# Performance work log

Hardware: AMD Instinct MI355X
Metric: run time of the kernel (lower is better)

The kernel has to match this reference:

```python
import jax, jax.numpy as jnp
import numpy as np

FP8_MAX = 448.0  # float8_e4m3fn max
EPS = 1e-6
H = 4096
T = 16384


def _rmsnorm(x, w, eps=EPS):
    # vLLM RMSNorm: x * rsqrt(mean(x^2) + eps) * weight, computed in fp32
    ms = jnp.mean(x * x, axis=-1, keepdims=True)
    return x * jax.lax.rsqrt(ms + eps) * w


def _fp8_linear_dyn(y, w_t, wscale):
    # per-token dynamic fp8 quant: scale = max|y| / 448, quantize, fp8 GEMM, dequant
    s = jnp.max(jnp.abs(y), axis=-1, keepdims=True) / FP8_MAX  # [T,1]
    s = jnp.maximum(s, 1e-10)
    q = jnp.clip(y / s, -FP8_MAX, FP8_MAX)
    q = q.astype(jnp.float8_e4m3fn).astype(jnp.float32)  # snap to fp8 grid
    out = q @ w_t                                         # [T,H]
    return out * s * wscale[:, 0]                          # per-token * per-out-channel


def setup_inputs() -> dict:
    key = jax.random.key(0)
    ks = jax.random.split(key, 9)
    x = jax.random.uniform(ks[0], (T, H), dtype=jnp.float32)
    # RMSNorm weights (init ones in vLLM; perturb for a nontrivial baseline)
    nw0 = 1.0 + 0.1 * jax.random.normal(ks[1], (H,), dtype=jnp.float32)
    nw1 = 1.0 + 0.1 * jax.random.normal(ks[2], (H,), dtype=jnp.float32)
    nw2 = 1.0 + 0.1 * jax.random.normal(ks[3], (H,), dtype=jnp.float32)
    # fp8 weights: rand(H,H) snapped to e4m3 grid, transposed (y @ W.T)
    def fp8_w(k):
        w = jax.random.uniform(k, (H, H), dtype=jnp.float32)
        return w.astype(jnp.float8_e4m3fn).astype(jnp.float32).T
    w0 = fp8_w(ks[4])
    w1 = fp8_w(ks[5])
    ws0 = jax.random.uniform(ks[6], (H, 1), dtype=jnp.float32)
    ws1 = jax.random.uniform(ks[7], (H, 1), dtype=jnp.float32)
    return {"x": x, "nw0": nw0, "nw1": nw1, "nw2": nw2,
            "w0": w0, "w1": w1, "ws0": ws0, "ws1": ws1}


def reference(x, nw0, nw1, nw2, w0, w1, ws0, ws1):
    resid = jnp.sqrt(x)
    y = _rmsnorm(x, nw0)
    x2 = _fp8_linear_dyn(y, w0, ws0)
    # fused add + rmsnorm: residual updated in place semantics
    resid = x2 + resid
    y2 = _rmsnorm(resid, nw1)
    x3 = _fp8_linear_dyn(y2, w1, ws1)
    resid = x3 + resid
    y3 = _rmsnorm(resid, nw2)
    return y3
```

## Files before the change

### kernel.cpp

```cpp
#include <hip/hip_runtime.h>
#include <stdint.h>

#define TT 16384
#define HH 4096

typedef uint8_t u8;
typedef uint32_t u32;
typedef __attribute__((ext_vector_type(16))) float f32x16;
typedef __attribute__((ext_vector_type(8))) int i32x8;

__device__ __forceinline__ u32 cvt4_fp8(float a, float b, float c, float d) {
  u32 v = 0;
  v = __builtin_amdgcn_cvt_pk_fp8_f32(a, b, v, false);
  v = __builtin_amdgcn_cvt_pk_fp8_f32(c, d, v, true);
  return v;
}

__device__ __forceinline__ void gl_lds16(const void* g, void* l) {
  __builtin_amdgcn_global_load_lds(
      (const __attribute__((address_space(1))) void*)g,
      (__attribute__((address_space(3))) void*)l, 16, 0, 0);
}

__device__ __forceinline__ i32x8 ld32B(const u8* p0, const u8* p1) {
  const uint4 a = *(const uint4*)p0;
  const uint4 b = *(const uint4*)p1;
  i32x8 r;
  r[0] = (int)a.x; r[1] = (int)a.y; r[2] = (int)a.z; r[3] = (int)a.w;
  r[4] = (int)b.x; r[5] = (int)b.y; r[6] = (int)b.z; r[7] = (int)b.w;
  return r;
}

__global__ __launch_bounds__(256) void kwquant(const float* __restrict__ w,
                                               u8* __restrict__ wq) {
  __shared__ __align__(16) u8 tile[64][68];
  const int n0 = blockIdx.x * 64;
  const int k0 = blockIdx.y * 64;
  const int t = threadIdx.x;
  const int tr = t >> 4, tc = t & 15;
#pragma unroll
  for (int p = 0; p < 4; ++p) {
    const int kl = p * 16 + tr;
    const float4 v = *(const float4*)(w + (size_t)(k0 + kl) * HH + n0 + tc * 4);
    const u32 pk = cvt4_fp8(v.x, v.y, v.z, v.w);
    tile[tc * 4 + 0][kl] = (u8)(pk);
    tile[tc * 4 + 1][kl] = (u8)(pk >> 8);
    tile[tc * 4 + 2][kl] = (u8)(pk >> 16);
    tile[tc * 4 + 3][kl] = (u8)(pk >> 24);
  }
  __syncthreads();
  const int jr = t >> 2;
  const int kc = (t & 3) * 16;
  uint4 ov;
  ov.x = *(const u32*)&tile[jr][kc + 0];
  ov.y = *(const u32*)&tile[jr][kc + 4];
  ov.z = *(const u32*)&tile[jr][kc + 8];
  ov.w = *(const u32*)&tile[jr][kc + 12];
  *(uint4*)(wq + (size_t)(n0 + jr) * HH + k0 + kc) = ov;
}

__device__ __forceinline__ float wred_sum(float v) {
#pragma unroll
  for (int o = 32; o; o >>= 1) v += __shfl_down(v, o, 64);
  return v;
}
__device__ __forceinline__ float wred_max(float v) {
#pragma unroll
  for (int o = 32; o; o >>= 1) v = fmaxf(v, __shfl_down(v, o, 64));
  return v;
}

template <int MODE>
__global__ __launch_bounds__(256) void knorm(const float* __restrict__ src,
                                             const float* __restrict__ nw,
                                             float* __restrict__ resid_out,
                                             u8* __restrict__ qout,
                                             float* __restrict__ sout,
                                             float* __restrict__ yout) {
  __shared__ float red[4];
  __shared__ float redm[4];
  const int row = blockIdx.x;
  const int t = threadIdx.x;
  const int lane = t & 63, wid = t >> 6;
  const float* rp = src + (size_t)row * HH;

  float4 xv[4];
  float ssq = 0.f;
#pragma unroll
  for (int p = 0; p < 4; ++p) {
    xv[p] = *((const float4*)rp + p * 256 + t);
    ssq += xv[p].x * xv[p].x;
    ssq += xv[p].y * xv[p].y;
    ssq += xv[p].z * xv[p].z;
    ssq += xv[p].w * xv[p].w;
  }
  if (MODE == 0) {
    float* rr = resid_out + (size_t)row * HH;
#pragma unroll
    for (int p = 0; p < 4; ++p) {
      float4 r4;
      r4.x = sqrtf(xv[p].x); r4.y = sqrtf(xv[p].y);
      r4.z = sqrtf(xv[p].z); r4.w = sqrtf(xv[p].w);
      *((float4*)rr + p * 256 + t) = r4;
    }
  }
  ssq = wred_sum(ssq);
  if (lane == 0) red[wid] = ssq;
  __syncthreads();
  const float ms = (((red[0] + red[1]) + red[2]) + red[3]) * (1.0f / HH);
  const float inv = 1.0f / sqrtf(ms + 1e-6f);

  float y[16];
  float amax = 0.f;
#pragma unroll
  for (int p = 0; p < 4; ++p) {
    const float4 wv = *((const float4*)nw + p * 256 + t);
    y[p * 4 + 0] = (xv[p].x * inv) * wv.x;
    y[p * 4 + 1] = (xv[p].y * inv) * wv.y;
    y[p * 4 + 2] = (xv[p].z * inv) * wv.z;
    y[p * 4 + 3] = (xv[p].w * inv) * wv.w;
    amax = fmaxf(amax, fabsf(y[p * 4 + 0]));
    amax = fmaxf(amax, fabsf(y[p * 4 + 1]));
    amax = fmaxf(amax, fabsf(y[p * 4 + 2]));
    amax = fmaxf(amax, fabsf(y[p * 4 + 3]));
  }

  if (MODE == 2) {
    float* yp = yout + (size_t)row * HH;
#pragma unroll
    for (int p = 0; p < 4; ++p) {
      float4 o;
      o.x = y[p * 4 + 0]; o.y = y[p * 4 + 1];
      o.z = y[p * 4 + 2]; o.w = y[p * 4 + 3];
      *((float4*)yp + p * 256 + t) = o;
    }
    return;
  }

  amax = wred_max(amax);
  if (lane == 0) redm[wid] = amax;
  __syncthreads();
  const float bmax = fmaxf(fmaxf(redm[0], redm[1]), fmaxf(redm[2], redm[3]));
  const float sval = fmaxf(bmax / 448.0f, 1e-10f);

  u32* qp = (u32*)(qout + (size_t)row * HH);
#pragma unroll
  for (int p = 0; p < 4; ++p) {
    float q0 = fminf(fmaxf(y[p * 4 + 0] / sval, -448.f), 448.f);
    float q1 = fminf(fmaxf(y[p * 4 + 1] / sval, -448.f), 448.f);
    float q2 = fminf(fmaxf(y[p * 4 + 2] / sval, -448.f), 448.f);
    float q3 = fminf(fmaxf(y[p * 4 + 3] / sval, -448.f), 448.f);
    qp[p * 256 + t] = cvt4_fp8(q0, q1, q2, q3);
  }
  if (t == 0) sout[row] = sval;
}

__global__ __launch_bounds__(512) void kgemm(const u8* __restrict__ Aq,
                                             const u8* __restrict__ Bq,
                                             const float* __restrict__ srow,
                                             const float* __restrict__ wsc,
                                             float* __restrict__ resid) {
  constexpr int K = HH, N = HH;
  constexpr int NT = K / 64;
  __shared__ __align__(16) u8 smA[2][256 * 64];
  __shared__ __align__(16) u8 smB[2][256 * 64];

  const int nwg = (TT / 256) * (HH / 256);
  int bid = blockIdx.x;
  bid = (bid & 7) * (nwg >> 3) + (bid >> 3);
  const int tm = bid >> 4;
  const int tn = bid & 15;
  const int row0 = tm * 256, col0 = tn * 256;

  const int t = threadIdx.x;
  const int lane = t & 63, wid = t >> 6;
  const int wm = wid >> 2, wn = wid & 3;
  const int rl32 = lane & 31, hi = lane >> 5;

  f32x16 acc[4][2];
#pragma unroll
  for (int m = 0; m < 4; ++m)
#pragma unroll
    for (int n = 0; n < 2; ++n) acc[m][n] = (f32x16)0.f;

  int aoffg[2], boffg[2], ldso[2];
#pragma unroll
  for (int p = 0; p < 2; ++p) {
    const int s = t + p * 512;
    const int r = s >> 2;
    const int cb = (s & 3) ^ ((r >> 1) & 3);
    aoffg[p] = (row0 + r) * K + cb * 16;
    boffg[p] = (col0 + r) * K + cb * 16;
    ldso[p] = s * 16;
  }

  int aro[4][2], bro[2][2];
#pragma unroll
  for (int m = 0; m < 4; ++m) {
    const int r = wm * 128 + m * 32 + rl32;
    const int swz = (r >> 1) & 3;
    aro[m][0] = r * 64 + ((hi * 2) ^ swz) * 16;
    aro[m][1] = r * 64 + ((hi * 2 + 1) ^ swz) * 16;
  }
#pragma unroll
  for (int n = 0; n < 2; ++n) {
    const int r = wn * 64 + n * 32 + rl32;
    const int swz = (r >> 1) & 3;
    bro[n][0] = r * 64 + ((hi * 2) ^ swz) * 16;
    bro[n][1] = r * 64 + ((hi * 2 + 1) ^ swz) * 16;
  }

#pragma unroll
  for (int p = 0; p < 2; ++p) {
    gl_lds16(Aq + aoffg[p], smA[0] + ldso[p]);
    gl_lds16(Bq + boffg[p], smB[0] + ldso[p]);
  }

  for (int it = 0; it < NT; ++it) {
    if (it + 1 < NT) {
      const size_t ko = (size_t)(it + 1) * 64;
      const int nb = (it + 1) & 1;
#pragma unroll
      for (int p = 0; p < 2; ++p) {
        gl_lds16(Aq + aoffg[p] + ko, smA[nb] + ldso[p]);
        gl_lds16(Bq + boffg[p] + ko, smB[nb] + ldso[p]);
      }
      asm volatile("s_waitcnt vmcnt(4)" ::: "memory");
    } else {
      asm volatile("s_waitcnt vmcnt(0)" ::: "memory");
    }
    __builtin_amdgcn_s_barrier();
    __builtin_amdgcn_sched_barrier(0);

    const u8* sA = smA[it & 1];
    const u8* sB = smB[it & 1];
    const i32x8 bv0 = ld32B(sB + bro[0][0], sB + bro[0][1]);
    const i32x8 bv1 = ld32B(sB + bro[1][0], sB + bro[1][1]);
#pragma unroll
    for (int m = 0; m < 4; ++m) {
      const i32x8 av = ld32B(sA + aro[m][0], sA + aro[m][1]);
      acc[m][0] = __builtin_amdgcn_mfma_scale_f32_32x32x64_f8f6f4(
          av, bv0, acc[m][0], 0 , 0 ,
          0, 0x7f7f7f7f, 0, 0x7f7f7f7f);
      acc[m][1] = __builtin_amdgcn_mfma_scale_f32_32x32x64_f8f6f4(
          av, bv1, acc[m][1], 0, 0, 0, 0x7f7f7f7f, 0, 0x7f7f7f7f);
    }
    __builtin_amdgcn_sched_barrier(0);
    __builtin_amdgcn_s_barrier();
  }

  const int cc = rl32;
  const int rb = hi * 4;
  float wvv[2];
#pragma unroll
  for (int n = 0; n < 2; ++n) wvv[n] = wsc[col0 + wn * 64 + n * 32 + cc];
#pragma unroll
  for (int m = 0; m < 4; ++m) {
#pragma unroll
    for (int g = 0; g < 4; ++g) {
#pragma unroll
      for (int j = 0; j < 4; ++j) {
        const int row = row0 + wm * 128 + m * 32 + g * 8 + rb + j;
        const float sv = srow[row];
#pragma unroll
        for (int n = 0; n < 2; ++n) {
          const int col = col0 + wn * 64 + n * 32 + cc;
          const size_t idx = (size_t)row * N + col;
          resid[idx] = resid[idx] + (acc[m][n][g * 4 + j] * sv) * wvv[n];
        }
      }
    }
  }
}

extern "C" void kernel_launch(void* const* d_in, const int* in_sizes, int n_in,
                              void* d_out, int out_size, void* d_ws, size_t ws_size,
                              hipStream_t stream) {
  const float* x   = (const float*)d_in[0];
  const float* nw0 = (const float*)d_in[1];
  const float* nw1 = (const float*)d_in[2];
  const float* nw2 = (const float*)d_in[3];
  const float* w0  = (const float*)d_in[4];
  const float* w1  = (const float*)d_in[5];
  const float* ws0 = (const float*)d_in[6];
  const float* ws1 = (const float*)d_in[7];
  float* out = (float*)d_out;

  u8* q = (u8*)d_ws;
  u8* w0q = q + (size_t)TT * HH;
  u8* w1q = w0q + (size_t)HH * HH;
  float* sbuf = (float*)(w1q + (size_t)HH * HH);

  dim3 wg(HH / 64, HH / 64);
  kwquant<<<wg, 256, 0, stream>>>(w0, w0q);
  kwquant<<<wg, 256, 0, stream>>>(w1, w1q);

  const int gblocks = (TT / 256) * (HH / 256);
  knorm<0><<<TT, 256, 0, stream>>>(x, nw0, out, q, sbuf, nullptr);
  kgemm<<<gblocks, 512, 0, stream>>>(q, w0q, sbuf, ws0, out);
  knorm<1><<<TT, 256, 0, stream>>>(out, nw1, nullptr, q, sbuf, nullptr);
  kgemm<<<gblocks, 512, 0, stream>>>(q, w1q, sbuf, ws1, out);
  knorm<2><<<TT, 256, 0, stream>>>(out, nw2, nullptr, nullptr, nullptr, out);
}
```

Baseline: 1.109 ms.

## Triple-buffer GEMM LDS and interleave global prefetch with MFMA phases

Replaces the double-buffered A/B shared-memory tiles with a three-stage ring buffer that prefetches two K-steps ahead. Global-to-LDS loads are split into four pieces, each issued inside one of four MFMA sub-phases with barriers and s_setprio around the matrix ops, so memory traffic overlaps compute. The workgroup-to-tile mapping is also changed to group 2x2 tile blocks per XCD for better L2 locality. In exchange it uses more LDS (96KB) and many more barriers per iteration, which could hurt occupancy or add sync overhead.

```diff
diff --git a/kernel.cpp b/kernel.cpp
--- a/kernel.cpp
+++ b/kernel.cpp
@@ -162,14 +162,16 @@
                                              float* __restrict__ resid) {
   constexpr int K = HH, N = HH;
   constexpr int NT = K / 64;
-  __shared__ __align__(16) u8 smA[2][256 * 64];
-  __shared__ __align__(16) u8 smB[2][256 * 64];
-
-  const int nwg = (TT / 256) * (HH / 256);
-  int bid = blockIdx.x;
-  bid = (bid & 7) * (nwg >> 3) + (bid >> 3);
-  const int tm = bid >> 4;
-  const int tn = bid & 15;
+  __shared__ __align__(16) u8 sm[3][32768];
+
+  const int bidraw = blockIdx.x;
+  const int xcd = bidraw & 7;
+  const int c = bidraw >> 3;
+  const int g = c >> 2;
+  const int gr = g >> 3, gc = g & 7;
+  const int gm = (c >> 1) & 1, gn = c & 1;
+  const int tm = xcd * 8 + gr * 2 + gm;
+  const int tn = gc * 2 + gn;
   const int row0 = tm * 256, col0 = tn * 256;
 
   const int t = threadIdx.x;
@@ -183,24 +185,21 @@
 #pragma unroll
     for (int n = 0; n < 2; ++n) acc[m][n] = (f32x16)0.f;
 
-  int aoffg[2], boffg[2], ldso[2];
-#pragma unroll
-  for (int p = 0; p < 2; ++p) {
-    const int s = t + p * 512;
-    const int r = s >> 2;
-    const int cb = (s & 3) ^ ((r >> 1) & 3);
-    aoffg[p] = (row0 + r) * K + cb * 16;
-    boffg[p] = (col0 + r) * K + cb * 16;
-    ldso[p] = s * 16;
-  }
+  const int sr = t >> 2;
+  const int scb = (t & 3) ^ ((sr >> 1) & 3);
+  const int gBlo = (col0 + sr) * K + scb * 16;
+  const int gBhi = (col0 + 128 + sr) * K + scb * 16;
+  const int gAlo = (row0 + sr) * K + scb * 16;
+  const int gAhi = (row0 + 128 + sr) * K + scb * 16;
+  const int dst = t * 16;
 
   int aro[4][2], bro[2][2];
 #pragma unroll
   for (int m = 0; m < 4; ++m) {
     const int r = wm * 128 + m * 32 + rl32;
     const int swz = (r >> 1) & 3;
-    aro[m][0] = r * 64 + ((hi * 2) ^ swz) * 16;
-    aro[m][1] = r * 64 + ((hi * 2 + 1) ^ swz) * 16;
+    aro[m][0] = 16384 + r * 64 + ((hi * 2) ^ swz) * 16;
+    aro[m][1] = 16384 + r * 64 + ((hi * 2 + 1) ^ swz) * 16;
   }
 #pragma unroll
   for (int n = 0; n < 2; ++n) {
@@ -210,43 +209,96 @@
     bro[n][1] = r * 64 + ((hi * 2 + 1) ^ swz) * 16;
   }
 
-#pragma unroll
-  for (int p = 0; p < 2; ++p) {
-    gl_lds16(Aq + aoffg[p], smA[0] + ldso[p]);
-    gl_lds16(Bq + boffg[p], smB[0] + ldso[p]);
-  }
+  gl_lds16(Bq + gBlo, sm[0] + dst);
+  gl_lds16(Bq + gBhi, sm[0] + 8192 + dst);
+  gl_lds16(Aq + gAlo, sm[0] + 16384 + dst);
+  gl_lds16(Aq + gAhi, sm[0] + 24576 + dst);
+  gl_lds16(Bq + gBlo + 64, sm[1] + dst);
+  gl_lds16(Bq + gBhi + 64, sm[1] + 8192 + dst);
+  gl_lds16(Aq + gAlo + 64, sm[1] + 16384 + dst);
+  gl_lds16(Aq + gAhi + 64, sm[1] + 24576 + dst);
+  asm volatile("s_waitcnt vmcnt(4)" ::: "memory");
+  __builtin_amdgcn_s_barrier();
+  __builtin_amdgcn_sched_barrier(0);
 
   for (int it = 0; it < NT; ++it) {
-    if (it + 1 < NT) {
-      const size_t ko = (size_t)(it + 1) * 64;
-      const int nb = (it + 1) & 1;
-#pragma unroll
-      for (int p = 0; p < 2; ++p) {
-        gl_lds16(Aq + aoffg[p] + ko, smA[nb] + ldso[p]);
-        gl_lds16(Bq + boffg[p] + ko, smB[nb] + ldso[p]);
+    const u8* sb = sm[it % 3];
+    u8* db = sm[(it + 2) % 3];
+    const bool st = (it + 2 < NT);
+    const int ko = (it + 2) * 64;
+    i32x8 bv0, bv1;
+
+    {
+      bv0 = ld32B(sb + bro[0][0], sb + bro[0][1]);
+      bv1 = ld32B(sb + bro[1][0], sb + bro[1][1]);
+      const i32x8 av = ld32B(sb + aro[0][0], sb + aro[0][1]);
+      if (st) gl_lds16(Bq + gBlo + ko, db + dst);
+      __builtin_amdgcn_sched_barrier(0);
+      __builtin_amdgcn_s_barrier();
+      asm volatile("s_waitcnt lgkmcnt(0)" ::: "memory");
+      __builtin_amdgcn_sched_barrier(0);
+      __builtin_amdgcn_s_setprio(1);
+      acc[0][0] = __builtin_amdgcn_mfma_scale_f32_32x32x64_f8f6f4(
+          av, bv0, acc[0][0], 0, 0, 0, 0x7f7f7f7f, 0, 0x7f7f7f7f);
+      acc[0][1] = __builtin_amdgcn_mfma_scale_f32_32x32x64_f8f6f4(
+          av, bv1, acc[0][1], 0, 0, 0, 0x7f7f7f7f, 0, 0x7f7f7f7f);
+      __builtin_amdgcn_s_setprio(0);
+      __builtin_amdgcn_sched_barrier(0);
+      __builtin_amdgcn_s_barrier();
+    }
+    {
+      const i32x8 av = ld32B(sb + aro[1][0], sb + aro[1][1]);
+      if (st) gl_lds16(Bq + gBhi + ko, db + 8192 + dst);
+      __builtin_amdgcn_sched_barrier(0);
+      __builtin_amdgcn_s_barrier();
+      asm volatile("s_waitcnt lgkmcnt(0)" ::: "memory");
+      __builtin_amdgcn_sched_barrier(0);
+      __builtin_amdgcn_s_setprio(1);
+      acc[1][0] = __builtin_amdgcn_mfma_scale_f32_32x32x64_f8f6f4(
+          av, bv0, acc[1][0], 0, 0, 0, 0x7f7f7f7f, 0, 0x7f7f7f7f);
+      acc[1][1] = __builtin_amdgcn_mfma_scale_f32_32x32x64_f8f6f4(
+          av, bv1, acc[1][1], 0, 0, 0, 0x7f7f7f7f, 0, 0x7f7f7f7f);
+      __builtin_amdgcn_s_setprio(0);
+      __builtin_amdgcn_sched_barrier(0);
+      __builtin_amdgcn_s_barrier();
+    }
+    {
+      const i32x8 av = ld32B(sb + aro[2][0], sb + aro[2][1]);
+      if (st) gl_lds16(Aq + gAlo + ko, db + 16384 + dst);
+      __builtin_amdgcn_sched_barrier(0);
+      __builtin_amdgcn_s_barrier();
+      asm volatile("s_waitcnt lgkmcnt(0)" ::: "memory");
+      __builtin_amdgcn_sched_barrier(0);
+      __builtin_amdgcn_s_setprio(1);
+      acc[2][0] = __builtin_amdgcn_mfma_scale_f32_32x32x64_f8f6f4(
+          av, bv0, acc[2][0], 0, 0, 0, 0x7f7f7f7f, 0, 0x7f7f7f7f);
+      acc[2][1] = __builtin_amdgcn_mfma_scale_f32_32x32x64_f8f6f4(
+          av, bv1, acc[2][1], 0, 0, 0, 0x7f7f7f7f, 0, 0x7f7f7f7f);
+      __builtin_amdgcn_s_setprio(0);
+      __builtin_amdgcn_sched_barrier(0);
+      __builtin_amdgcn_s_barrier();
+    }
+    {
+      const i32x8 av = ld32B(sb + aro[3][0], sb + aro[3][1]);
+      if (st) gl_lds16(Aq + gAhi + ko, db + 24576 + dst);
+      __builtin_amdgcn_sched_barrier(0);
+      __builtin_amdgcn_s_barrier();
+      asm volatile("s_waitcnt lgkmcnt(0)" ::: "memory");
+      __builtin_amdgcn_sched_barrier(0);
+      __builtin_amdgcn_s_setprio(1);
+      acc[3][0] = __builtin_amdgcn_mfma_scale_f32_32x32x64_f8f6f4(
+          av, bv0, acc[3][0], 0, 0, 0, 0x7f7f7f7f, 0, 0x7f7f7f7f);
+      acc[3][1] = __builtin_amdgcn_mfma_scale_f32_32x32x64_f8f6f4(
+          av, bv1, acc[3][1], 0, 0, 0, 0x7f7f7f7f, 0, 0x7f7f7f7f);
+      __builtin_amdgcn_s_setprio(0);
+      if (st) {
+        asm volatile("s_waitcnt vmcnt(4)" ::: "memory");
+      } else {
+        asm volatile("s_waitcnt vmcnt(0)" ::: "memory");
       }
-      asm volatile("s_waitcnt vmcnt(4)" ::: "memory");
-    } else {
-      asm volatile("s_waitcnt vmcnt(0)" ::: "memory");
-    }
-    __builtin_amdgcn_s_barrier();
-    __builtin_amdgcn_sched_barrier(0);
-
-    const u8* sA = smA[it & 1];
-    const u8* sB = smB[it & 1];
-    const i32x8 bv0 = ld32B(sB + bro[0][0], sB + bro[0][1]);
-    const i32x8 bv1 = ld32B(sB + bro[1][0], sB + bro[1][1]);
-#pragma unroll
-    for (int m = 0; m < 4; ++m) {
-      const i32x8 av = ld32B(sA + aro[m][0], sA + aro[m][1]);
-      acc[m][0] = __builtin_amdgcn_mfma_scale_f32_32x32x64_f8f6f4(
-          av, bv0, acc[m][0], 0 , 0 ,
-          0, 0x7f7f7f7f, 0, 0x7f7f7f7f);
-      acc[m][1] = __builtin_amdgcn_mfma_scale_f32_32x32x64_f8f6f4(
-          av, bv1, acc[m][1], 0, 0, 0, 0x7f7f7f7f, 0, 0x7f7f7f7f);
-    }
-    __builtin_amdgcn_sched_barrier(0);
-    __builtin_amdgcn_s_barrier();
+      __builtin_amdgcn_sched_barrier(0);
+      __builtin_amdgcn_s_barrier();
+    }
   }
 
   const int cc = rl32;
@@ -257,16 +309,16 @@
 #pragma unroll
   for (int m = 0; m < 4; ++m) {
 #pragma unroll
-    for (int g = 0; g < 4; ++g) {
+    for (int g2 = 0; g2 < 4; ++g2) {
 #pragma unroll
       for (int j = 0; j < 4; ++j) {
-        const int row = row0 + wm * 128 + m * 32 + g * 8 + rb + j;
+        const int row = row0 + wm * 128 + m * 32 + g2 * 8 + rb + j;
         const float sv = srow[row];
 #pragma unroll
         for (int n = 0; n < 2; ++n) {
           const int col = col0 + wn * 64 + n * 32 + cc;
           const size_t idx = (size_t)row * N + col;
-          resid[idx] = resid[idx] + (acc[m][n][g * 4 + j] * sv) * wvv[n];
+          resid[idx] = resid[idx] + (acc[m][n][g2 * 4 + j] * sv) * wvv[n];
         }
       }
     }
```

Measured after the change: 1.216 ms. +9.6%, slower.

## Retile FP8 GEMM to 128x128 blocks with triple-buffered LDS pipeline

Applied to the files above, without the earlier changes.

Replaces the 256x256 tile, 8-wave GEMM with a 128x128 tile, 2-wave block. Loads are triple buffered with a prefetch distance of two k-steps. The block-to-tile mapping now groups tiles by XCD for L2 locality, and the MFMA section runs at raised wave priority. The aim is higher occupancy and better latency hiding, at the cost of less data reuse per block and more global traffic for the A and B tiles.

```diff
diff --git a/kernel.cpp b/kernel.cpp
--- a/kernel.cpp
+++ b/kernel.cpp
@@ -155,26 +155,28 @@
   if (t == 0) sout[row] = sval;
 }
 
-__global__ __launch_bounds__(512) void kgemm(const u8* __restrict__ Aq,
+__global__ __launch_bounds__(128) void kgemm(const u8* __restrict__ Aq,
                                              const u8* __restrict__ Bq,
                                              const float* __restrict__ srow,
                                              const float* __restrict__ wsc,
                                              float* __restrict__ resid) {
   constexpr int K = HH, N = HH;
   constexpr int NT = K / 64;
-  __shared__ __align__(16) u8 smA[2][256 * 64];
-  __shared__ __align__(16) u8 smB[2][256 * 64];
-
-  const int nwg = (TT / 256) * (HH / 256);
-  int bid = blockIdx.x;
-  bid = (bid & 7) * (nwg >> 3) + (bid >> 3);
-  const int tm = bid >> 4;
-  const int tn = bid & 15;
-  const int row0 = tm * 256, col0 = tn * 256;
+  __shared__ __align__(16) u8 sm[3][16384];
+
+  const int bidraw = blockIdx.x;
+  const int xcd = bidraw & 7;
+  const int c = bidraw >> 3;
+  const int g = c >> 4;
+  const int gr = g >> 3, gc = g & 7;
+  const int gm = (c >> 2) & 3, gn = c & 3;
+  const int tm = xcd * 16 + gr * 4 + gm;
+  const int tn = gc * 4 + gn;
+  const int row0 = tm * 128, col0 = tn * 128;
 
   const int t = threadIdx.x;
-  const int lane = t & 63, wid = t >> 6;
-  const int wm = wid >> 2, wn = wid & 3;
+  const int lane = t & 63;
+  const int wn = t >> 6;
   const int rl32 = lane & 31, hi = lane >> 5;
 
   f32x16 acc[4][2];
@@ -183,68 +185,67 @@
 #pragma unroll
     for (int n = 0; n < 2; ++n) acc[m][n] = (f32x16)0.f;
 
-  int aoffg[2], boffg[2], ldso[2];
-#pragma unroll
-  for (int p = 0; p < 2; ++p) {
-    const int s = t + p * 512;
-    const int r = s >> 2;
-    const int cb = (s & 3) ^ ((r >> 1) & 3);
-    aoffg[p] = (row0 + r) * K + cb * 16;
-    boffg[p] = (col0 + r) * K + cb * 16;
-    ldso[p] = s * 16;
+  int goff[8];
+#pragma unroll
+  for (int p = 0; p < 8; ++p) {
+    const int slot = (p & 3) * 128 + t;
+    const int r = slot >> 2;
+    const int cb = (slot & 3) ^ (r & 3);
+    goff[p] = ((p < 4 ? row0 : col0) + r) * K + cb * 16;
   }
 
   int aro[4][2], bro[2][2];
 #pragma unroll
   for (int m = 0; m < 4; ++m) {
-    const int r = wm * 128 + m * 32 + rl32;
-    const int swz = (r >> 1) & 3;
+    const int r = m * 32 + rl32;
+    const int swz = r & 3;
     aro[m][0] = r * 64 + ((hi * 2) ^ swz) * 16;
     aro[m][1] = r * 64 + ((hi * 2 + 1) ^ swz) * 16;
   }
 #pragma unroll
   for (int n = 0; n < 2; ++n) {
     const int r = wn * 64 + n * 32 + rl32;
-    const int swz = (r >> 1) & 3;
-    bro[n][0] = r * 64 + ((hi * 2) ^ swz) * 16;
-    bro[n][1] = r * 64 + ((hi * 2 + 1) ^ swz) * 16;
-  }
-
-#pragma unroll
-  for (int p = 0; p < 2; ++p) {
-    gl_lds16(Aq + aoffg[p], smA[0] + ldso[p]);
-    gl_lds16(Bq + boffg[p], smB[0] + ldso[p]);
-  }
+    const int swz = r & 3;
+    bro[n][0] = 8192 + r * 64 + ((hi * 2) ^ swz) * 16;
+    bro[n][1] = 8192 + r * 64 + ((hi * 2 + 1) ^ swz) * 16;
+  }
+
+#pragma unroll
+  for (int p = 0; p < 8; ++p)
+    gl_lds16((p < 4 ? Aq : Bq) + goff[p], sm[0] + p * 2048 + t * 16);
+#pragma unroll
+  for (int p = 0; p < 8; ++p)
+    gl_lds16((p < 4 ? Aq : Bq) + goff[p] + 64, sm[1] + p * 2048 + t * 16);
 
   for (int it = 0; it < NT; ++it) {
-    if (it + 1 < NT) {
-      const size_t ko = (size_t)(it + 1) * 64;
-      const int nb = (it + 1) & 1;
-#pragma unroll
-      for (int p = 0; p < 2; ++p) {
-        gl_lds16(Aq + aoffg[p] + ko, smA[nb] + ldso[p]);
-        gl_lds16(Bq + boffg[p] + ko, smB[nb] + ldso[p]);
-      }
-      asm volatile("s_waitcnt vmcnt(4)" ::: "memory");
+    const u8* sb = sm[it % 3];
+    u8* db = sm[(it + 2) % 3];
+    if (it + 2 < NT) {
+      const int ko = (it + 2) * 64;
+#pragma unroll
+      for (int p = 0; p < 8; ++p)
+        gl_lds16((p < 4 ? Aq : Bq) + goff[p] + ko, db + p * 2048 + t * 16);
+      asm volatile("s_waitcnt vmcnt(16)" ::: "memory");
+    } else if (it + 1 < NT) {
+      asm volatile("s_waitcnt vmcnt(8)" ::: "memory");
     } else {
       asm volatile("s_waitcnt vmcnt(0)" ::: "memory");
     }
     __builtin_amdgcn_s_barrier();
     __builtin_amdgcn_sched_barrier(0);
 
-    const u8* sA = smA[it & 1];
-    const u8* sB = smB[it & 1];
-    const i32x8 bv0 = ld32B(sB + bro[0][0], sB + bro[0][1]);
-    const i32x8 bv1 = ld32B(sB + bro[1][0], sB + bro[1][1]);
+    const i32x8 bv0 = ld32B(sb + bro[0][0], sb + bro[0][1]);
+    const i32x8 bv1 = ld32B(sb + bro[1][0], sb + bro[1][1]);
+    __builtin_amdgcn_s_setprio(1);
 #pragma unroll
     for (int m = 0; m < 4; ++m) {
-      const i32x8 av = ld32B(sA + aro[m][0], sA + aro[m][1]);
+      const i32x8 av = ld32B(sb + aro[m][0], sb + aro[m][1]);
       acc[m][0] = __builtin_amdgcn_mfma_scale_f32_32x32x64_f8f6f4(
-          av, bv0, acc[m][0], 0 , 0 ,
-          0, 0x7f7f7f7f, 0, 0x7f7f7f7f);
+          av, bv0, acc[m][0], 0, 0, 0, 0x7f7f7f7f, 0, 0x7f7f7f7f);
       acc[m][1] = __builtin_amdgcn_mfma_scale_f32_32x32x64_f8f6f4(
           av, bv1, acc[m][1], 0, 0, 0, 0x7f7f7f7f, 0, 0x7f7f7f7f);
     }
+    __builtin_amdgcn_s_setprio(0);
     __builtin_amdgcn_sched_barrier(0);
     __builtin_amdgcn_s_barrier();
   }
@@ -257,16 +258,16 @@
 #pragma unroll
   for (int m = 0; m < 4; ++m) {
 #pragma unroll
-    for (int g = 0; g < 4; ++g) {
+    for (int g2 = 0; g2 < 4; ++g2) {
 #pragma unroll
       for (int j = 0; j < 4; ++j) {
-        const int row = row0 + wm * 128 + m * 32 + g * 8 + rb + j;
+        const int row = row0 + m * 32 + g2 * 8 + rb + j;
         const float sv = srow[row];
 #pragma unroll
         for (int n = 0; n < 2; ++n) {
           const int col = col0 + wn * 64 + n * 32 + cc;
           const size_t idx = (size_t)row * N + col;
-          resid[idx] = resid[idx] + (acc[m][n][g * 4 + j] * sv) * wvv[n];
+          resid[idx] = resid[idx] + (acc[m][n][g2 * 4 + j] * sv) * wvv[n];
         }
       }
     }
@@ -295,10 +296,9 @@
   kwquant<<<wg, 256, 0, stream>>>(w0, w0q);
   kwquant<<<wg, 256, 0, stream>>>(w1, w1q);
 
-  const int gblocks = (TT / 256) * (HH / 256);
   knorm<0><<<TT, 256, 0, stream>>>(x, nw0, out, q, sbuf, nullptr);
-  kgemm<<<gblocks, 512, 0, stream>>>(q, w0q, sbuf, ws0, out);
+  kgemm<<<(TT / 128) * (HH / 128), 128, 0, stream>>>(q, w0q, sbuf, ws0, out);
   knorm<1><<<TT, 256, 0, stream>>>(out, nw1, nullptr, q, sbuf, nullptr);
-  kgemm<<<gblocks, 512, 0, stream>>>(q, w1q, sbuf, ws1, out);
+  kgemm<<<(TT / 128) * (HH / 128), 128, 0, stream>>>(q, w1q, sbuf, ws1, out);
   knorm<2><<<TT, 256, 0, stream>>>(out, nw2, nullptr, nullptr, nullptr, out);
 }
```

Measured after the change: 1.134 ms. 1.02x slower.
